# Kernel optimization log

Measured on AMD Instinct MI355X. Metric: run time of the kernel, lower is better.

The kernel has to match this reference:

```python
import jax, jax.numpy as jnp
import numpy as np

B, N_ANT, M_MEAS, D_A, MAX_ITER = 1024, 64, 16, 4096, 20
SC_L = 10


def setup_inputs() -> dict:
    key = jax.random.key(0)
    ks = jax.random.split(key, 9)
    return {
        "x_re": jax.random.normal(ks[0], (B, M_MEAS), jnp.float32),
        "x_im": jax.random.normal(ks[1], (B, M_MEAS), jnp.float32),
        "xm_re": jax.random.normal(ks[2], (B, N_ANT), jnp.float32),
        "xm_im": jax.random.normal(ks[3], (B, N_ANT), jnp.float32),
        "M_re": jax.random.normal(ks[4], (B, N_ANT, M_MEAS), jnp.float32),
        "M_im": jax.random.normal(ks[5], (B, N_ANT, M_MEAS), jnp.float32),
        "W_re": jax.random.normal(ks[6], (N_ANT, D_A), jnp.float32),
        "W_im": jax.random.normal(ks[7], (N_ANT, D_A), jnp.float32),
        "sigma": jax.random.uniform(ks[8], (B,), jnp.float32) * 0.05,
        "L": SC_L,
        "k": 1,
    }


def _mpnet_forward(x, xm, M, W, sigma, L):
    # M_D[b] = conj(M[b]^T) @ W  -> [B, m, d_a]
    M_D = jnp.einsum('bnm,na->bma', jnp.conj(M), W)
    # per-sample column normalization (norms are constants: torch computes them on detached numpy)
    md_norm = jax.lax.stop_gradient(
        jnp.sqrt(jnp.sum(jnp.abs(M_D) ** 2, axis=1, keepdims=True)))  # [B,1,d_a]
    M_D = M_D / md_norm
    e_norm = jax.lax.stop_gradient(
        jnp.sqrt(jnp.sum(jnp.abs(W) ** 2, axis=0, keepdims=True)))  # [1,d_a]
    E = W / e_norm  # [N, d_a]

    n_full = xm.shape[1]
    threshold = (sigma ** 2) * n_full * L  # sc == 2

    def body(carry, _):
        residual, res, active = carry
        rn2 = jnp.sum(jnp.abs(residual) ** 2, axis=1)         # [B]
        active = active & (rn2 >= threshold)                  # per-sample early exit
        corr = jnp.einsum('bm,bma->ba', residual, jnp.conj(M_D))  # [B,d_a]
        idx = jnp.argmax(jnp.abs(corr), axis=1)               # top-1 (keep_k_max, k=1)
        val = jnp.take_along_axis(corr, idx[:, None], axis=1)           # [B,1]
        col = jnp.take_along_axis(M_D, idx[:, None, None], axis=2)[..., 0]  # [B,m]
        colE = jnp.take(E, idx, axis=1).T                     # [B,N]
        residual = jnp.where(active[:, None], residual - val * col, residual)
        res = jnp.where(active[:, None], res - val * colE, res)
        return (residual, res, active), None

    init = (x, xm, jnp.ones((x.shape[0],), dtype=bool))
    (residual, res, _), _ = jax.lax.scan(body, init, None, length=MAX_ITER)
    x_hat = x - residual
    x_hat_m = xm - res
    return residual, x_hat, x_hat_m


def reference(x_re, x_im, xm_re, xm_im, M_re, M_im, W_re, W_im, sigma, L, k):
    x = (x_re + 1j * x_im).astype(jnp.complex64)
    xm = (xm_re + 1j * xm_im).astype(jnp.complex64)
    M = (M_re + 1j * M_im).astype(jnp.complex64)
    W = (W_re + 1j * W_im).astype(jnp.complex64)
    return _mpnet_forward(x, xm, M, W, sigma, L)
```

## Files before the change

### kernel.cpp

```cpp
#include <hip/hip_runtime.h>
#include <cstdint>
#include <cstddef>

#define NB_TOT 1024
#define NANT 64
#define MM 16
#define MPAD 17
#define DA 4096
#define MAXIT 20
#define SPB 4
#define NTHR 1024
#define JCOLS 4
#define L_CONST 10.0f

__global__ __launch_bounds__(NTHR, 4)
void mpnet_kernel(const float* __restrict__ x_re, const float* __restrict__ x_im,
                  const float* __restrict__ xm_re, const float* __restrict__ xm_im,
                  const float* __restrict__ M_re, const float* __restrict__ M_im,
                  const float* __restrict__ W_re, const float* __restrict__ W_im,
                  const float* __restrict__ sigma,
                  float* __restrict__ out, int outn_i)
{
  __shared__ float Msh_re[SPB][NANT][MPAD];
  __shared__ float Msh_im[SPB][NANT][MPAD];
  __shared__ float md_T[SPB][JCOLS][NTHR];
  __shared__ float tsh[NANT][8];
  __shared__ float rsd_re[SPB][MM], rsd_im[SPB][MM];
  __shared__ float resh_re[SPB][NANT], resh_im[SPB][NANT];
  __shared__ float red_c2[16][SPB];
  __shared__ int   red_ix[16][SPB];
  __shared__ float rn2_sh[SPB], thr_sh[SPB];
  __shared__ int   actsh[SPB];

  const int tid = threadIdx.x;
  const int b0 = blockIdx.x * SPB;
  const size_t outn = (size_t)outn_i;

  for (int k2 = 0; k2 < 4; k2++){
    int idx = k2*NTHR + tid;
    int s = idx >> 10, rem = idx & 1023;
    int n = rem >> 4, m = rem & 15;
    Msh_re[s][n][m] = M_re[(size_t)b0*1024 + idx];
    Msh_im[s][n][m] = M_im[(size_t)b0*1024 + idx];
  }
  if (tid < SPB*MM){
    int s = tid >> 4, m = tid & 15;
    rsd_re[s][m] = x_re[(b0+s)*MM + m];
    rsd_im[s][m] = x_im[(b0+s)*MM + m];
  } else if (tid >= 64 && tid < 64 + SPB*NANT){
    int q = tid - 64, s = q >> 6, n = q & 63;
    resh_re[s][n] = xm_re[(b0+s)*NANT + n];
    resh_im[s][n] = xm_im[(b0+s)*NANT + n];
  } else if (tid >= 448 && tid < 448 + SPB){
    int s = tid - 448;
    float sg = sigma[b0+s];
    thr_sh[s] = ((sg*sg) * (float)NANT) * L_CONST;
    actsh[s] = 1;
  }

  #pragma unroll
  for (int s = 0; s < SPB; s++){
    const float* MrS = M_re + (size_t)(b0+s)*1024;
    const float* MiS = M_im + (size_t)(b0+s)*1024;
    #pragma unroll
    for (int jc = 0; jc < JCOLS; jc++){
      const int col = (tid<<2) + jc;
      float cr[MM], ci[MM];
      #pragma unroll
      for (int q = 0; q < MM; q++){ cr[q]=0.f; ci[q]=0.f; }
      #pragma unroll 2
      for (int n = 0; n < NANT; n++){
        float wr = W_re[(size_t)n*DA + col];
        float wi = W_im[(size_t)n*DA + col];
        const float* Mr = MrS + n*MM;
        const float* Mi = MiS + n*MM;
        #pragma unroll
        for (int q2 = 0; q2 < 4; q2++){
          float4 m4r = *(const float4*)(Mr + q2*4);
          float4 m4i = *(const float4*)(Mi + q2*4);
          cr[q2*4+0] += m4r.x*wr + m4i.x*wi;  ci[q2*4+0] += m4r.x*wi - m4i.x*wr;
          cr[q2*4+1] += m4r.y*wr + m4i.y*wi;  ci[q2*4+1] += m4r.y*wi - m4i.y*wr;
          cr[q2*4+2] += m4r.z*wr + m4i.z*wi;  ci[q2*4+2] += m4r.z*wi - m4i.z*wr;
          cr[q2*4+3] += m4r.w*wr + m4i.w*wi;  ci[q2*4+3] += m4r.w*wi - m4i.w*wr;
        }
      }
      float nrm = 0.f;
      #pragma unroll
      for (int q = 0; q < MM; q++) nrm += cr[q]*cr[q] + ci[q]*ci[q];
      md_T[s][jc][tid] = 1.f/sqrtf(nrm);
    }
  }
  __syncthreads();

  for (int it = 0; it < MAXIT; it++){
    if (tid < SPB){
      float e = 0.f;
      #pragma unroll
      for (int m = 0; m < MM; m++){
        float rr = rsd_re[tid][m], ri = rsd_im[tid][m];
        e += rr*rr + ri*ri;
      }
      rn2_sh[tid] = e;
    } else if (tid >= 64 && tid < 320){
      int q = tid - 64, s = q >> 6, n = q & 63;
      if (actsh[s]){
        float tr = 0.f, ti = 0.f;
        #pragma unroll
        for (int m = 0; m < MM; m++){
          float mr = Msh_re[s][n][m], mi = Msh_im[s][n][m];
          float rr = rsd_re[s][m], ri = rsd_im[s][m];
          tr += mr*rr - mi*ri;
          ti += mr*ri + mi*rr;
        }
        tsh[n][2*s]   = tr;
        tsh[n][2*s+1] = ti;
      }
    }
    __syncthreads();

    bool a0 = actsh[0] && (rn2_sh[0] >= thr_sh[0]);
    bool a1 = actsh[1] && (rn2_sh[1] >= thr_sh[1]);
    bool a2 = actsh[2] && (rn2_sh[2] >= thr_sh[2]);
    bool a3 = actsh[3] && (rn2_sh[3] >= thr_sh[3]);
    if (tid < 4){
      int v = (tid==0) ? (int)a0 : (tid==1) ? (int)a1 : (tid==2) ? (int)a2 : (int)a3;
      actsh[tid] = v;
    }
    if (!(a0 || a1 || a2 || a3)) break;

    float gr[SPB][JCOLS], gi[SPB][JCOLS];
    #pragma unroll
    for (int s = 0; s < SPB; s++)
      #pragma unroll
      for (int j = 0; j < JCOLS; j++){ gr[s][j]=0.f; gi[s][j]=0.f; }
    #pragma unroll 8
    for (int n = 0; n < NANT; n++){
      float4 t01 = *(const float4*)&tsh[n][0];
      float4 t23 = *(const float4*)&tsh[n][4];
      float4 wr = *(const float4*)(W_re + (size_t)n*DA + (tid<<2));
      float4 wi = *(const float4*)(W_im + (size_t)n*DA + (tid<<2));
      if (a0){
        gr[0][0] += wr.x*t01.x + wi.x*t01.y;  gi[0][0] += wr.x*t01.y - wi.x*t01.x;
        gr[0][1] += wr.y*t01.x + wi.y*t01.y;  gi[0][1] += wr.y*t01.y - wi.y*t01.x;
        gr[0][2] += wr.z*t01.x + wi.z*t01.y;  gi[0][2] += wr.z*t01.y - wi.z*t01.x;
        gr[0][3] += wr.w*t01.x + wi.w*t01.y;  gi[0][3] += wr.w*t01.y - wi.w*t01.x;
      }
      if (a1){
        gr[1][0] += wr.x*t01.z + wi.x*t01.w;  gi[1][0] += wr.x*t01.w - wi.x*t01.z;
        gr[1][1] += wr.y*t01.z + wi.y*t01.w;  gi[1][1] += wr.y*t01.w - wi.y*t01.z;
        gr[1][2] += wr.z*t01.z + wi.z*t01.w;  gi[1][2] += wr.z*t01.w - wi.z*t01.z;
        gr[1][3] += wr.w*t01.z + wi.w*t01.w;  gi[1][3] += wr.w*t01.w - wi.w*t01.z;
      }
      if (a2){
        gr[2][0] += wr.x*t23.x + wi.x*t23.y;  gi[2][0] += wr.x*t23.y - wi.x*t23.x;
        gr[2][1] += wr.y*t23.x + wi.y*t23.y;  gi[2][1] += wr.y*t23.y - wi.y*t23.x;
        gr[2][2] += wr.z*t23.x + wi.z*t23.y;  gi[2][2] += wr.z*t23.y - wi.z*t23.x;
        gr[2][3] += wr.w*t23.x + wi.w*t23.y;  gi[2][3] += wr.w*t23.y - wi.w*t23.x;
      }
      if (a3){
        gr[3][0] += wr.x*t23.z + wi.x*t23.w;  gi[3][0] += wr.x*t23.w - wi.x*t23.z;
        gr[3][1] += wr.y*t23.z + wi.y*t23.w;  gi[3][1] += wr.y*t23.w - wi.y*t23.z;
        gr[3][2] += wr.z*t23.z + wi.z*t23.w;  gi[3][2] += wr.z*t23.w - wi.z*t23.z;
        gr[3][3] += wr.w*t23.z + wi.w*t23.w;  gi[3][3] += wr.w*t23.w - wi.w*t23.z;
      }
    }

    const bool acts[4] = {a0, a1, a2, a3};
    float bc2[SPB]; int bix[SPB];
    #pragma unroll
    for (int s = 0; s < SPB; s++){
      bc2[s] = -1.f; bix[s] = 0;
      if (acts[s]){
        float m0 = md_T[s][0][tid], m1 = md_T[s][1][tid];
        float m2 = md_T[s][2][tid], m3 = md_T[s][3][tid];
        float c0 = (gr[s][0]*gr[s][0] + gi[s][0]*gi[s][0]) * (m0*m0);
        float c1 = (gr[s][1]*gr[s][1] + gi[s][1]*gi[s][1]) * (m1*m1);
        float c2v = (gr[s][2]*gr[s][2] + gi[s][2]*gi[s][2]) * (m2*m2);
        float c3 = (gr[s][3]*gr[s][3] + gi[s][3]*gi[s][3]) * (m3*m3);
        float bc = c0; int bi = (tid<<2);
        if (c1 > bc){ bc = c1; bi = (tid<<2)+1; }
        if (c2v > bc){ bc = c2v; bi = (tid<<2)+2; }
        if (c3 > bc){ bc = c3; bi = (tid<<2)+3; }
        bc2[s] = bc; bix[s] = bi;
      }
    }
    #pragma unroll
    for (int s = 0; s < SPB; s++){
      if (acts[s]){
        #pragma unroll
        for (int off = 32; off; off >>= 1){
          float oc2 = __shfl_down(bc2[s], off);
          int   oix = __shfl_down(bix[s], off);
          if (oc2 > bc2[s] || (oc2 == bc2[s] && oix < bix[s])){ bc2[s]=oc2; bix[s]=oix; }
        }
      }
    }
    if ((tid & 63) == 0){
      int wid = tid >> 6;
      #pragma unroll
      for (int s = 0; s < SPB; s++){
        if (acts[s]){ red_c2[wid][s]=bc2[s]; red_ix[wid][s]=bix[s]; }
      }
    }
    __syncthreads();

    if (tid < 256){
      int s = tid >> 6, lane = tid & 63;
      if (actsh[s]){
        float c = (lane < 16) ? red_c2[lane][s] : -1.f;
        int   bi = (lane < 16) ? red_ix[lane][s] : 0x7FFFFFFF;
        #pragma unroll
        for (int off = 8; off; off >>= 1){
          float oc = __shfl_xor(c, off);
          int   oi = __shfl_xor(bi, off);
          if (oc > c || (oc == c && oi < bi)){ c = oc; bi = oi; }
        }
        int I = __shfl(bi, 0);
        float wr = W_re[(size_t)lane*DA + I], wi = W_im[(size_t)lane*DA + I];
        float tr = tsh[lane][2*s], ti = tsh[lane][2*s+1];
        float vr = wr*tr + wi*ti;
        float vi = wr*ti - wi*tr;
        float w2 = wr*wr + wi*wi;
        #pragma unroll
        for (int off = 32; off; off >>= 1){
          vr += __shfl_xor(vr, off);
          vi += __shfl_xor(vi, off);
          w2 += __shfl_xor(w2, off);
        }
        float mdv = md_T[s][I & 3][I >> 2];
        float val_r = vr*mdv, val_i = vi*mdv;
        float einv = rsqrtf(w2);
        float er = wr*einv, em = wi*einv;
        resh_re[s][lane] -= val_r*er - val_i*em;
        resh_im[s][lane] -= val_r*em + val_i*er;
        for (int m = 0; m < MM; m++){
          float mr = Msh_re[s][lane][m], mi = Msh_im[s][lane][m];
          float pr = mr*wr + mi*wi;
          float pi = mr*wi - mi*wr;
          #pragma unroll
          for (int off = 32; off; off >>= 1){
            pr += __shfl_xor(pr, off);
            pi += __shfl_xor(pi, off);
          }
          if (lane == m){
            float col_r = pr*mdv, col_i = pi*mdv;
            rsd_re[s][m] -= val_r*col_r - val_i*col_i;
            rsd_im[s][m] -= val_r*col_i + val_i*col_r;
          }
        }
      }
    }
    __syncthreads();
  }

  if (tid < 64){
    int s = tid >> 4, m = tid & 15; int b = b0 + s;
    float rr = rsd_re[s][m], ri = rsd_im[s][m];
    size_t base = (size_t)b*MM + m;
    if (base < outn)          out[base]          = rr;
    if (16384 + base < outn)  out[16384 + base]  = x_re[b*MM+m] - rr;
    if (98304 + base < outn)  out[98304 + base]  = ri;
    if (114688 + base < outn) out[114688 + base] = x_im[b*MM+m] - ri;
  } else if (tid >= 64 && tid < 320){
    int q = tid - 64, s = q >> 6, n = q & 63; int b = b0 + s;
    size_t base = (size_t)b*NANT + n;
    if (32768 + base < outn)  out[32768 + base]  = xm_re[b*NANT+n] - resh_re[s][n];
    if (131072 + base < outn) out[131072 + base] = xm_im[b*NANT+n] - resh_im[s][n];
  }
}

extern "C" void kernel_launch(void* const* d_in, const int* in_sizes, int n_in,
                              void* d_out, int out_size, void* d_ws, size_t ws_size,
                              hipStream_t stream) {
  (void)in_sizes; (void)n_in; (void)d_ws; (void)ws_size;
  const float* x_re  = (const float*)d_in[0];
  const float* x_im  = (const float*)d_in[1];
  const float* xm_re = (const float*)d_in[2];
  const float* xm_im = (const float*)d_in[3];
  const float* M_re  = (const float*)d_in[4];
  const float* M_im  = (const float*)d_in[5];
  const float* W_re  = (const float*)d_in[6];
  const float* W_im  = (const float*)d_in[7];
  const float* sig   = (const float*)d_in[8];
  float* out = (float*)d_out;

  dim3 grid(NB_TOT / SPB), block(NTHR);
  hipLaunchKernelGGL(mpnet_kernel, grid, block, 0, stream,
                     x_re, x_im, xm_re, xm_im, M_re, M_im, W_re, W_im,
                     sig, out, out_size);
}
```

Before: 1.418 ms.

## Precompute per-sample column inverse norms in a separate kernel and recompute correlations on the fly

Splits the work into a precompute kernel and a loop kernel. The precompute kernel fills a workspace with the inverse column norms of conj(M)^T W, one per sample and column. The loop kernel reassociates each iteration's correlation as W^H (M r), scaled by that stored norm, so the normalized M_D matrix is never held in shared memory. It also picks the argmax on squared magnitudes and rebuilds the chosen column directly from M and W. This frees the large md_T shared buffer, which may allow more blocks per CU, but it re-reads W from global memory every iteration, and the old fused kernel is kept as a fallback when the workspace is too small.

Result: no change. 1.436 ms (+1.3%).

```diff
diff --git a/kernel.cpp b/kernel.cpp
--- a/kernel.cpp
+++ b/kernel.cpp
@@ -12,9 +12,271 @@
 #define NTHR 1024
 #define JCOLS 4
 #define L_CONST 10.0f
+#define MD_BYTES ((size_t)NB_TOT * DA * sizeof(float))
+
+__global__ __launch_bounds__(256, 8)
+void md_kernel(const float* __restrict__ M_re, const float* __restrict__ M_im,
+               const float* __restrict__ W_re, const float* __restrict__ W_im,
+               float* __restrict__ md_ws)
+{
+  const int b   = blockIdx.x >> 1;
+  const int h   = blockIdx.x & 1;
+  const int tid = threadIdx.x;
+  const float* MrS = M_re + (size_t)b*1024;
+  const float* MiS = M_im + (size_t)b*1024;
+
+  #pragma unroll
+  for (int k = 0; k < 8; k++){
+    const int col = h*2048 + k*256 + tid;
+    float cr[MM], ci[MM];
+    #pragma unroll
+    for (int q = 0; q < MM; q++){ cr[q]=0.f; ci[q]=0.f; }
+    #pragma unroll 2
+    for (int n = 0; n < NANT; n++){
+      float wr = W_re[(size_t)n*DA + col];
+      float wi = W_im[(size_t)n*DA + col];
+      const float* Mr = MrS + n*MM;
+      const float* Mi = MiS + n*MM;
+      #pragma unroll
+      for (int q2 = 0; q2 < 4; q2++){
+        float4 m4r = *(const float4*)(Mr + q2*4);
+        float4 m4i = *(const float4*)(Mi + q2*4);
+        cr[q2*4+0] += m4r.x*wr + m4i.x*wi;  ci[q2*4+0] += m4r.x*wi - m4i.x*wr;
+        cr[q2*4+1] += m4r.y*wr + m4i.y*wi;  ci[q2*4+1] += m4r.y*wi - m4i.y*wr;
+        cr[q2*4+2] += m4r.z*wr + m4i.z*wi;  ci[q2*4+2] += m4r.z*wi - m4i.z*wr;
+        cr[q2*4+3] += m4r.w*wr + m4i.w*wi;  ci[q2*4+3] += m4r.w*wi - m4i.w*wr;
+      }
+    }
+    float nrm = 0.f;
+    #pragma unroll
+    for (int q = 0; q < MM; q++) nrm += cr[q]*cr[q] + ci[q]*ci[q];
+    md_ws[(size_t)b*DA + col] = 1.f/sqrtf(nrm);
+  }
+}
 
 __global__ __launch_bounds__(NTHR, 4)
-void mpnet_kernel(const float* __restrict__ x_re, const float* __restrict__ x_im,
+void loop_kernel(const float* __restrict__ x_re, const float* __restrict__ x_im,
+                 const float* __restrict__ xm_re, const float* __restrict__ xm_im,
+                 const float* __restrict__ M_re, const float* __restrict__ M_im,
+                 const float* __restrict__ W_re, const float* __restrict__ W_im,
+                 const float* __restrict__ sigma, const float* __restrict__ md_ws,
+                 float* __restrict__ out, int outn_i)
+{
+  __shared__ float Msh_re[SPB][NANT][MPAD];
+  __shared__ float Msh_im[SPB][NANT][MPAD];
+  __shared__ float tsh[NANT][8];
+  __shared__ float rsd_re[SPB][MM], rsd_im[SPB][MM];
+  __shared__ float resh_re[SPB][NANT], resh_im[SPB][NANT];
+  __shared__ float red_c2[16][SPB];
+  __shared__ int   red_ix[16][SPB];
+  __shared__ float rn2_sh[SPB], thr_sh[SPB];
+  __shared__ int   actsh[SPB];
+
+  const int tid = threadIdx.x;
+  const int b0 = blockIdx.x * SPB;
+  const size_t outn = (size_t)outn_i;
+
+  for (int k2 = 0; k2 < 4; k2++){
+    int idx = k2*NTHR + tid;
+    int s = idx >> 10, rem = idx & 1023;
+    int n = rem >> 4, m = rem & 15;
+    Msh_re[s][n][m] = M_re[(size_t)b0*1024 + idx];
+    Msh_im[s][n][m] = M_im[(size_t)b0*1024 + idx];
+  }
+  if (tid < SPB*MM){
+    int s = tid >> 4, m = tid & 15;
+    rsd_re[s][m] = x_re[(b0+s)*MM + m];
+    rsd_im[s][m] = x_im[(b0+s)*MM + m];
+  } else if (tid >= 64 && tid < 64 + SPB*NANT){
+    int q = tid - 64, s = q >> 6, n = q & 63;
+    resh_re[s][n] = xm_re[(b0+s)*NANT + n];
+    resh_im[s][n] = xm_im[(b0+s)*NANT + n];
+  } else if (tid >= 448 && tid < 448 + SPB){
+    int s = tid - 448;
+    float sg = sigma[b0+s];
+    thr_sh[s] = ((sg*sg) * (float)NANT) * L_CONST;
+    actsh[s] = 1;
+  }
+  __syncthreads();
+
+  for (int it = 0; it < MAXIT; it++){
+    if (tid < SPB){
+      float e = 0.f;
+      #pragma unroll
+      for (int m = 0; m < MM; m++){
+        float rr = rsd_re[tid][m], ri = rsd_im[tid][m];
+        e += rr*rr + ri*ri;
+      }
+      rn2_sh[tid] = e;
+    } else if (tid >= 64 && tid < 320){
+      int q = tid - 64, s = q >> 6, n = q & 63;
+      if (actsh[s]){
+        float tr = 0.f, ti = 0.f;
+        #pragma unroll
+        for (int m = 0; m < MM; m++){
+          float mr = Msh_re[s][n][m], mi = Msh_im[s][n][m];
+          float rr = rsd_re[s][m], ri = rsd_im[s][m];
+          tr += mr*rr - mi*ri;
+          ti += mr*ri + mi*rr;
+        }
+        tsh[n][2*s]   = tr;
+        tsh[n][2*s+1] = ti;
+      }
+    }
+    __syncthreads();
+
+    bool a0 = actsh[0] && (rn2_sh[0] >= thr_sh[0]);
+    bool a1 = actsh[1] && (rn2_sh[1] >= thr_sh[1]);
+    bool a2 = actsh[2] && (rn2_sh[2] >= thr_sh[2]);
+    bool a3 = actsh[3] && (rn2_sh[3] >= thr_sh[3]);
+    if (tid < 4){
+      int v = (tid==0) ? (int)a0 : (tid==1) ? (int)a1 : (tid==2) ? (int)a2 : (int)a3;
+      actsh[tid] = v;
+    }
+    if (!(a0 || a1 || a2 || a3)) break;
+
+    float gr[SPB][JCOLS], gi[SPB][JCOLS];
+    #pragma unroll
+    for (int s = 0; s < SPB; s++)
+      #pragma unroll
+      for (int j = 0; j < JCOLS; j++){ gr[s][j]=0.f; gi[s][j]=0.f; }
+    #pragma unroll 8
+    for (int n = 0; n < NANT; n++){
+      float4 t01 = *(const float4*)&tsh[n][0];
+      float4 t23 = *(const float4*)&tsh[n][4];
+      float4 wr = *(const float4*)(W_re + (size_t)n*DA + (tid<<2));
+      float4 wi = *(const float4*)(W_im + (size_t)n*DA + (tid<<2));
+      if (a0){
+        gr[0][0] += wr.x*t01.x + wi.x*t01.y;  gi[0][0] += wr.x*t01.y - wi.x*t01.x;
+        gr[0][1] += wr.y*t01.x + wi.y*t01.y;  gi[0][1] += wr.y*t01.y - wi.y*t01.x;
+        gr[0][2] += wr.z*t01.x + wi.z*t01.y;  gi[0][2] += wr.z*t01.y - wi.z*t01.x;
+        gr[0][3] += wr.w*t01.x + wi.w*t01.y;  gi[0][3] += wr.w*t01.y - wi.w*t01.x;
+      }
+      if (a1){
+        gr[1][0] += wr.x*t01.z + wi.x*t01.w;  gi[1][0] += wr.x*t01.w - wi.x*t01.z;
+        gr[1][1] += wr.y*t01.z + wi.y*t01.w;  gi[1][1] += wr.y*t01.w - wi.y*t01.z;
+        gr[1][2] += wr.z*t01.z + wi.z*t01.w;  gi[1][2] += wr.z*t01.w - wi.z*t01.z;
+        gr[1][3] += wr.w*t01.z + wi.w*t01.w;  gi[1][3] += wr.w*t01.w - wi.w*t01.z;
+      }
+      if (a2){
+        gr[2][0] += wr.x*t23.x + wi.x*t23.y;  gi[2][0] += wr.x*t23.y - wi.x*t23.x;
+        gr[2][1] += wr.y*t23.x + wi.y*t23.y;  gi[2][1] += wr.y*t23.y - wi.y*t23.x;
+        gr[2][2] += wr.z*t23.x + wi.z*t23.y;  gi[2][2] += wr.z*t23.y - wi.z*t23.x;
+        gr[2][3] += wr.w*t23.x + wi.w*t23.y;  gi[2][3] += wr.w*t23.y - wi.w*t23.x;
+      }
+      if (a3){
+        gr[3][0] += wr.x*t23.z + wi.x*t23.w;  gi[3][0] += wr.x*t23.w - wi.x*t23.z;
+        gr[3][1] += wr.y*t23.z + wi.y*t23.w;  gi[3][1] += wr.y*t23.w - wi.y*t23.z;
+        gr[3][2] += wr.z*t23.z + wi.z*t23.w;  gi[3][2] += wr.z*t23.w - wi.z*t23.z;
+        gr[3][3] += wr.w*t23.z + wi.w*t23.w;  gi[3][3] += wr.w*t23.w - wi.w*t23.z;
+      }
+    }
+
+    const bool acts[4] = {a0, a1, a2, a3};
+    float bc2[SPB]; int bix[SPB];
+    #pragma unroll
+    for (int s = 0; s < SPB; s++){
+      bc2[s] = -1.f; bix[s] = 0;
+      if (acts[s]){
+        float4 md4 = *(const float4*)(md_ws + (size_t)(b0+s)*DA + (tid<<2));
+        float c0 = (gr[s][0]*gr[s][0] + gi[s][0]*gi[s][0]) * (md4.x*md4.x);
+        float c1 = (gr[s][1]*gr[s][1] + gi[s][1]*gi[s][1]) * (md4.y*md4.y);
+        float c2v = (gr[s][2]*gr[s][2] + gi[s][2]*gi[s][2]) * (md4.z*md4.z);
+        float c3 = (gr[s][3]*gr[s][3] + gi[s][3]*gi[s][3]) * (md4.w*md4.w);
+        float bc = c0; int bi = (tid<<2);
+        if (c1 > bc){ bc = c1; bi = (tid<<2)+1; }
+        if (c2v > bc){ bc = c2v; bi = (tid<<2)+2; }
+        if (c3 > bc){ bc = c3; bi = (tid<<2)+3; }
+        bc2[s] = bc; bix[s] = bi;
+      }
+    }
+    #pragma unroll
+    for (int s = 0; s < SPB; s++){
+      if (acts[s]){
+        #pragma unroll
+        for (int off = 32; off; off >>= 1){
+          float oc2 = __shfl_down(bc2[s], off);
+          int   oix = __shfl_down(bix[s], off);
+          if (oc2 > bc2[s] || (oc2 == bc2[s] && oix < bix[s])){ bc2[s]=oc2; bix[s]=oix; }
+        }
+      }
+    }
+    if ((tid & 63) == 0){
+      int wid = tid >> 6;
+      #pragma unroll
+      for (int s = 0; s < SPB; s++){
+        if (acts[s]){ red_c2[wid][s]=bc2[s]; red_ix[wid][s]=bix[s]; }
+      }
+    }
+    __syncthreads();
+
+    if (tid < 256){
+      int s = tid >> 6, lane = tid & 63;
+      if (actsh[s]){
+        float c = (lane < 16) ? red_c2[lane][s] : -1.f;
+        int   bi = (lane < 16) ? red_ix[lane][s] : 0x7FFFFFFF;
+        #pragma unroll
+        for (int off = 8; off; off >>= 1){
+          float oc = __shfl_xor(c, off);
+          int   oi = __shfl_xor(bi, off);
+          if (oc > c || (oc == c && oi < bi)){ c = oc; bi = oi; }
+        }
+        int I = __shfl(bi, 0);
+        float wr = W_re[(size_t)lane*DA + I], wi = W_im[(size_t)lane*DA + I];
+        float tr = tsh[lane][2*s], ti = tsh[lane][2*s+1];
+        float vr = wr*tr + wi*ti;
+        float vi = wr*ti - wi*tr;
+        float w2 = wr*wr + wi*wi;
+        #pragma unroll
+        for (int off = 32; off; off >>= 1){
+          vr += __shfl_xor(vr, off);
+          vi += __shfl_xor(vi, off);
+          w2 += __shfl_xor(w2, off);
+        }
+        float mdv = md_ws[(size_t)(b0+s)*DA + I];
+        float val_r = vr*mdv, val_i = vi*mdv;
+        float einv = rsqrtf(w2);
+        float er = wr*einv, em = wi*einv;
+        resh_re[s][lane] -= val_r*er - val_i*em;
+        resh_im[s][lane] -= val_r*em + val_i*er;
+        for (int m = 0; m < MM; m++){
+          float mr = Msh_re[s][lane][m], mi = Msh_im[s][lane][m];
+          float pr = mr*wr + mi*wi;
+          float pi = mr*wi - mi*wr;
+          #pragma unroll
+          for (int off = 32; off; off >>= 1){
+            pr += __shfl_xor(pr, off);
+            pi += __shfl_xor(pi, off);
+          }
+          if (lane == m){
+            float col_r = pr*mdv, col_i = pi*mdv;
+            rsd_re[s][m] -= val_r*col_r - val_i*col_i;
+            rsd_im[s][m] -= val_r*col_i + val_i*col_r;
+          }
+        }
+      }
+    }
+    __syncthreads();
+  }
+
+  if (tid < 64){
+    int s = tid >> 4, m = tid & 15; int b = b0 + s;
+    float rr = rsd_re[s][m], ri = rsd_im[s][m];
+    size_t base = (size_t)b*MM + m;
+    if (base < outn)          out[base]          = rr;
+    if (16384 + base < outn)  out[16384 + base]  = x_re[b*MM+m] - rr;
+    if (98304 + base < outn)  out[98304 + base]  = ri;
+    if (114688 + base < outn) out[114688 + base] = x_im[b*MM+m] - ri;
+  } else if (tid >= 64 && tid < 320){
+    int q = tid - 64, s = q >> 6, n = q & 63; int b = b0 + s;
+    size_t base = (size_t)b*NANT + n;
+    if (32768 + base < outn)  out[32768 + base]  = xm_re[b*NANT+n] - resh_re[s][n];
+    if (131072 + base < outn) out[131072 + base] = xm_im[b*NANT+n] - resh_im[s][n];
+  }
+}
+
+__global__ __launch_bounds__(NTHR, 4)
+void fused_kernel(const float* __restrict__ x_re, const float* __restrict__ x_im,
                   const float* __restrict__ xm_re, const float* __restrict__ xm_im,
                   const float* __restrict__ M_re, const float* __restrict__ M_im,
                   const float* __restrict__ W_re, const float* __restrict__ W_im,
@@ -272,7 +534,7 @@
 extern "C" void kernel_launch(void* const* d_in, const int* in_sizes, int n_in,
                               void* d_out, int out_size, void* d_ws, size_t ws_size,
                               hipStream_t stream) {
-  (void)in_sizes; (void)n_in; (void)d_ws; (void)ws_size;
+  (void)in_sizes; (void)n_in;
   const float* x_re  = (const float*)d_in[0];
   const float* x_im  = (const float*)d_in[1];
   const float* xm_re = (const float*)d_in[2];
@@ -284,8 +546,16 @@
   const float* sig   = (const float*)d_in[8];
   float* out = (float*)d_out;
 
-  dim3 grid(NB_TOT / SPB), block(NTHR);
-  hipLaunchKernelGGL(mpnet_kernel, grid, block, 0, stream,
-                     x_re, x_im, xm_re, xm_im, M_re, M_im, W_re, W_im,
-                     sig, out, out_size);
+  if (ws_size >= MD_BYTES && d_ws != nullptr){
+    float* md_ws = (float*)d_ws;
+    hipLaunchKernelGGL(md_kernel, dim3(2048), dim3(256), 0, stream,
+                       M_re, M_im, W_re, W_im, md_ws);
+    hipLaunchKernelGGL(loop_kernel, dim3(NB_TOT / SPB), dim3(NTHR), 0, stream,
+                       x_re, x_im, xm_re, xm_im, M_re, M_im, W_re, W_im,
+                       sig, md_ws, out, out_size);
+  } else {
+    hipLaunchKernelGGL(fused_kernel, dim3(NB_TOT / SPB), dim3(NTHR), 0, stream,
+                       x_re, x_im, xm_re, xm_im, M_re, M_im, W_re, W_im,
+                       sig, out, out_size);
+  }
 }
```
